# Kernel optimization log

Measured on AMD Instinct MI355X. Metric: run time of the kernel, lower is better.

## Reference

```python
import jax, jax.numpy as jnp
import numpy as np

N_HEADS = 3
DS_ITERS = 20
EPS = 1e-8
LN_EPS = 1e-5


def rmsnorm(x, w):
    rms = jnp.sqrt(jnp.mean(x * x, axis=-1, keepdims=True) + EPS)
    return x / rms * w


def layernorm(x, w, b):
    m = jnp.mean(x, axis=-1, keepdims=True)
    v = jnp.mean((x - m) ** 2, axis=-1, keepdims=True)
    return (x - m) / jnp.sqrt(v + LN_EPS) * w + b


def sinkhorn(m):
    # m: [b, t, n, n]; global max-shift then exp, 20 alternating row/col normalizations
    m = m - jnp.max(m, axis=(-2, -1), keepdims=True)
    m = jnp.exp(m)
    def body(_, m):
        m = m / (jnp.sum(m, axis=-1, keepdims=True) + EPS)
        m = m / (jnp.sum(m, axis=-2, keepdims=True) + EPS)
        return m
    return jax.lax.fori_loop(0, DS_ITERS, body, m)


def encoder_block(x, ln1_w, ln1_b, Wq, Wk, Wv, Wo, ln2_w, ln2_b, W1, W2):
    # Standard pre-norm ViT encoder block, bias=False, dropout inactive (eval)
    b, t, d = x.shape
    hd = d // N_HEADS
    h = layernorm(x, ln1_w, ln1_b)
    q = (h @ Wq).reshape(b, t, N_HEADS, hd)
    k = (h @ Wk).reshape(b, t, N_HEADS, hd)
    v = (h @ Wv).reshape(b, t, N_HEADS, hd)
    scores = jnp.einsum('bqhd,bkhd->bhqk', q, k) / jnp.sqrt(jnp.asarray(hd, x.dtype))
    attn = jax.nn.softmax(scores, axis=-1)
    o = jnp.einsum('bhqk,bkhd->bqhd', attn, v).reshape(b, t, d) @ Wo
    x = x + o
    h2 = layernorm(x, ln2_w, ln2_b)
    x = x + jax.nn.gelu(h2 @ W1) @ W2
    return x


def setup_inputs() -> dict:
    key = jax.random.key(0)
    ks = jax.random.split(key, 12)
    b, t, n, d = 32, 1024, 4, 192
    nd, mlp = n * d, 768
    std = 0.02
    x = jax.random.normal(ks[0], (b, t, n, d), dtype=jnp.float32)
    b_res = jnp.full((n, n), -10.0, dtype=jnp.float32)
    b_res = b_res.at[jnp.arange(n), jnp.arange(n)].set(0.0)
    return {
        'x': x,
        'norm_w': jnp.ones((nd,), jnp.float32),
        'phi_pre': std * jax.random.normal(ks[1], (nd, n), jnp.float32),
        'phi_post': std * jax.random.normal(ks[2], (nd, n), jnp.float32),
        'phi_res': std * jax.random.normal(ks[3], (nd, n * n), jnp.float32),
        'b_pre': jnp.full((n,), float(np.log(1.0 / (n - 1.0))), jnp.float32),
        'b_post': jnp.zeros((n,), jnp.float32),
        'b_res': b_res,
        'alpha_pre': jnp.asarray(0.001, jnp.float32),
        'alpha_post': jnp.asarray(0.001, jnp.float32),
        'alpha_res': jnp.asarray(0.001, jnp.float32),
        'ln1_w': jnp.ones((d,), jnp.float32),
        'ln1_b': jnp.zeros((d,), jnp.float32),
        'Wq': std * jax.random.normal(ks[4], (d, d), jnp.float32),
        'Wk': std * jax.random.normal(ks[5], (d, d), jnp.float32),
        'Wv': std * jax.random.normal(ks[6], (d, d), jnp.float32),
        'Wo': std * jax.random.normal(ks[7], (d, d), jnp.float32),
        'ln2_w': jnp.ones((d,), jnp.float32),
        'ln2_b': jnp.zeros((d,), jnp.float32),
        'W1': std * jax.random.normal(ks[8], (d, mlp), jnp.float32),
        'W2': std * jax.random.normal(ks[9], (mlp, d), jnp.float32),
    }


def reference(x, norm_w, phi_pre, phi_post, phi_res, b_pre, b_post, b_res,
              alpha_pre, alpha_post, alpha_res,
              ln1_w, ln1_b, Wq, Wk, Wv, Wo, ln2_w, ln2_b, W1, W2):
    b, t, n, d = x.shape
    streams = rmsnorm(x.reshape(b, t, n * d), norm_w)
    pre_tilde = alpha_pre * (streams @ phi_pre) + b_pre              # [b,t,n]
    post_tilde = alpha_post * (streams @ phi_post) + b_post         # [b,t,n]
    res_tilde = alpha_res * (streams @ phi_res) + b_res.reshape(1, 1, n * n)
    h_pre = jax.nn.sigmoid(pre_tilde)
    h_post = 2.0 * jax.nn.sigmoid(post_tilde)
    h_res = sinkhorn(res_tilde.reshape(b, t, n, n))                 # doubly stochastic
    x_res = jnp.einsum('btij,btjd->btid', h_res, x)
    x_in = jnp.einsum('btn,btnd->btd', h_pre, x)
    y = encoder_block(x_in, ln1_w, ln1_b, Wq, Wk, Wv, Wo, ln2_w, ln2_b, W1, W2)
    x_out = y[:, :, None, :] * h_post[..., None]
    return x_res + x_out
```

## Files before the change

### kernel.cpp

```cpp
#include <hip/hip_runtime.h>
#include <hip/hip_bf16.h>
#include <math.h>

#define BATCH 32
#define SEQ   1024
#define NS    4
#define DIM   192
#define ND    768
#define NH    3
#define HD    64
#define MLP   768
#define TOKENS (BATCH*SEQ)

typedef __bf16 bf16;
typedef bf16  bf16x8 __attribute__((ext_vector_type(8)));
typedef bf16  bf16x4 __attribute__((ext_vector_type(4)));
typedef float f32x4  __attribute__((ext_vector_type(4)));

#define MFMA16(a,b,c) __builtin_amdgcn_mfma_f32_16x16x32_bf16(a,b,c,0,0,0)
#define LOG2E 1.44269504088896f

__device__ inline float gelu_tanh(float x) {
    float x3 = x * x * x;
    return 0.5f * x * (1.0f + tanhf(0.7978845608028654f * (x + 0.044715f * x3)));
}

__global__ __launch_bounds__(256) void wprep_kernel(
    const float* __restrict__ Wq, const float* __restrict__ Wk,
    const float* __restrict__ Wv, const float* __restrict__ Wo,
    const float* __restrict__ W1, const float* __restrict__ W2,
    const float* __restrict__ nw, const float* __restrict__ ppre,
    const float* __restrict__ ppost, const float* __restrict__ pres,
    bf16* __restrict__ wqkv, bf16* __restrict__ wot,
    bf16* __restrict__ w1t, bf16* __restrict__ w2t, bf16* __restrict__ phiw)
{
    const int z = blockIdx.z;
    const int tid = blockIdx.x * 256 + threadIdx.x;
    if (z == 6) {
        if (tid >= 32 * 96) return;
        const int n = tid / 96, k8 = tid % 96;
        const int kch = k8 >> 2, quad = k8 & 3;
        const int ntile = n >> 4, nc = n & 15;
        bf16* d = phiw + ((size_t)(ntile * 24 + kch) * 64 + quad * 16 + nc) * 8;
#pragma unroll
        for (int e = 0; e < 8; e++) {
            const int k = k8 * 8 + e;
            float v;
            if      (n < 4)  v = ppre [k * 4  + n];
            else if (n < 8)  v = ppost[k * 4  + n - 4];
            else if (n < 24) v = pres [k * 16 + n - 8];
            else             v = 0.f;
            d[e] = (bf16)(nw[k] * v);
        }
        return;
    }
    const float* src; bf16* dst; int K, N; float scale = 1.f;
    switch (z) {
        case 0: src = Wq; dst = wqkv;            K = 192; N = 192;
                scale = 0.125f * LOG2E; break;
        case 1: src = Wk; dst = wqkv + 36864;    K = 192; N = 192; break;
        case 2: src = Wv; dst = wqkv + 73728;    K = 192; N = 192; break;
        case 3: src = Wo; dst = wot;             K = 192; N = 192; break;
        case 4: src = W1; dst = w1t;             K = 192; N = 768; break;
        default:src = W2; dst = w2t;             K = 768; N = 192; break;
    }
    const int K8 = K >> 3, KC = K >> 5;
    if (tid >= N * K8) return;
    const int n = tid / K8, k8 = tid % K8;
    const int kch = k8 >> 2, quad = k8 & 3;
    const int ntile = n >> 4, nc = n & 15;
    bf16* d = dst + ((size_t)(ntile * KC + kch) * 64 + quad * 16 + nc) * 8;
#pragma unroll
    for (int e = 0; e < 8; e++)
        d[e] = (bf16)(scale * src[(size_t)(k8 * 8 + e) * N + n]);
}

__global__ __launch_bounds__(64) void prep_kernel(
    const float* __restrict__ x, bf16* __restrict__ xb, float* __restrict__ rinv)
{
    const int tok = blockIdx.x, lane = threadIdx.x;
    const float* xt = x + (size_t)tok * ND;
    float4 xv[3];
    float ssq = 0.f;
#pragma unroll
    for (int r = 0; r < 3; r++) {
        xv[r] = ((const float4*)xt)[lane + 64 * r];
        ssq += xv[r].x*xv[r].x + xv[r].y*xv[r].y + xv[r].z*xv[r].z + xv[r].w*xv[r].w;
    }
#pragma unroll
    for (int off = 32; off; off >>= 1) ssq += __shfl_xor(ssq, off);
    if (lane == 0) rinv[tok] = rsqrtf(ssq / (float)ND + 1e-8f);
#pragma unroll
    for (int r = 0; r < 3; r++) {
        bf16x4 o = {(bf16)xv[r].x, (bf16)xv[r].y, (bf16)xv[r].z, (bf16)xv[r].w};
        *(bf16x4*)(xb + (size_t)tok * ND + 4 * (lane + 64 * r)) = o;
    }
}

__global__ __launch_bounds__(256) void dots_kernel(
    const bf16* __restrict__ xb, const bf16* __restrict__ phiw,
    const float* __restrict__ rinv, float* __restrict__ dots)
{
    const int tid = threadIdx.x, lane = tid & 63, w = tid >> 6;
    const int quad = lane >> 4, c = lane & 15;
    const int tok0 = blockIdx.x * 64 + w * 16;

    f32x4 acc0 = {0.f,0.f,0.f,0.f}, acc1 = {0.f,0.f,0.f,0.f};
    const bf16* arow = xb + (size_t)(tok0 + c) * ND + quad * 8;
    const bf16* bbase = phiw + lane * 8;
#pragma unroll 6
    for (int k0 = 0; k0 < ND; k0 += 32) {
        const int kch = k0 >> 5;
        bf16x8 af  = *(const bf16x8*)(arow + k0);
        bf16x8 bf0 = *(const bf16x8*)(bbase + (size_t)kch * 512);
        bf16x8 bf1 = *(const bf16x8*)(bbase + (size_t)(24 + kch) * 512);
        acc0 = MFMA16(af, bf0, acc0);
        acc1 = MFMA16(af, bf1, acc1);
    }
#pragma unroll
    for (int r = 0; r < 4; r++) {
        const int tok = tok0 + quad * 4 + r;
        const float s = rinv[tok];
        dots[(size_t)tok * 32 + c]      = acc0[r] * s;
        dots[(size_t)tok * 32 + 16 + c] = acc1[r] * s;
    }
}

__global__ __launch_bounds__(256) void sink_kernel(
    const float* __restrict__ dots, const float* __restrict__ b_pre,
    const float* __restrict__ b_post, const float* __restrict__ b_res,
    const float* __restrict__ a_pre, const float* __restrict__ a_post,
    const float* __restrict__ a_res,
    float* __restrict__ hgate, float* __restrict__ hpost)
{
    const int tok = blockIdx.x * 256 + threadIdx.x;
    const float* dt = dots + (size_t)tok * 32;
    float d[24];
#pragma unroll
    for (int i = 0; i < 6; i++) *(float4*)&d[i*4] = *(const float4*)(dt + i*4);

    const float apre = a_pre[0], apost = a_post[0], ares = a_res[0];
    float hpre[4], hpo[4], m[16];
#pragma unroll
    for (int i = 0; i < 4; i++) {
        hpre[i] = 1.f / (1.f + __expf(-(apre  * d[i]     + b_pre[i])));
        hpo[i]  = 2.f / (1.f + __expf(-(apost * d[4 + i] + b_post[i])));
    }
#pragma unroll
    for (int p = 0; p < 16; p++) m[p] = ares * d[8 + p] + b_res[p];

    float gm = m[0];
#pragma unroll
    for (int p = 1; p < 16; p++) gm = fmaxf(gm, m[p]);
#pragma unroll
    for (int p = 0; p < 16; p++) m[p] = __expf(m[p] - gm);

    for (int it = 0; it < 20; it++) {
#pragma unroll
        for (int i = 0; i < 4; i++) {
            const float inv = 1.f / (m[i*4+0] + m[i*4+1] + m[i*4+2] + m[i*4+3] + 1e-8f);
#pragma unroll
            for (int j = 0; j < 4; j++) m[i*4+j] *= inv;
        }
#pragma unroll
        for (int j = 0; j < 4; j++) {
            const float inv = 1.f / (m[0*4+j] + m[1*4+j] + m[2*4+j] + m[3*4+j] + 1e-8f);
#pragma unroll
            for (int i = 0; i < 4; i++) m[i*4+j] *= inv;
        }
    }

    float* hg = hgate + (size_t)tok * 20;
#pragma unroll
    for (int i = 0; i < 4; i++) *(float4*)(hg + i*4) = *(float4*)&m[i*4];
    *(float4*)(hg + 16) = *(float4*)hpre;
    *(float4*)(hpost + (size_t)tok * 4) = *(float4*)hpo;
}

__global__ __launch_bounds__(64) void mix_kernel(
    const bf16* __restrict__ xb, const float* __restrict__ hgate,
    const float* __restrict__ ln1_w, const float* __restrict__ ln1_b,
    float* __restrict__ xin, bf16* __restrict__ h1)
{
    const int tok = blockIdx.x, lane = threadIdx.x;
    __shared__ float ldsx[ND];

    const bf16* xt = xb + (size_t)tok * ND;
#pragma unroll
    for (int r = 0; r < 3; r++) {
        const bf16x4 v = *(const bf16x4*)(xt + 4 * (lane + 64 * r));
        float4 f = {(float)v[0], (float)v[1], (float)v[2], (float)v[3]};
        ((float4*)ldsx)[lane + 64 * r] = f;
    }

    const float* hg = hgate + (size_t)tok * 20 + 16;
    float hpre[4];
#pragma unroll
    for (int i = 0; i < 4; i++) hpre[i] = hg[i];

    __syncthreads();

    float xi[3];
#pragma unroll
    for (int r = 0; r < 3; r++) {
        const int d = lane + 64 * r;
        xi[r] = hpre[0]*ldsx[d] + hpre[1]*ldsx[DIM+d]
              + hpre[2]*ldsx[2*DIM+d] + hpre[3]*ldsx[3*DIM+d];
    }
    float sum = xi[0] + xi[1] + xi[2];
#pragma unroll
    for (int off = 32; off; off >>= 1) sum += __shfl_xor(sum, off);
    const float mean = sum / (float)DIM;
    float vs = (xi[0]-mean)*(xi[0]-mean) + (xi[1]-mean)*(xi[1]-mean) + (xi[2]-mean)*(xi[2]-mean);
#pragma unroll
    for (int off = 32; off; off >>= 1) vs += __shfl_xor(vs, off);
    const float inv = rsqrtf(vs / (float)DIM + 1e-5f);

    float* xint = xin + (size_t)tok * DIM;
    bf16*  ht   = h1  + (size_t)tok * DIM;
#pragma unroll
    for (int r = 0; r < 3; r++) {
        const int d = lane + 64 * r;
        xint[d] = xi[r];
        ht[d]   = (bf16)((xi[r] - mean) * inv * ln1_w[d] + ln1_b[d]);
    }
}

template<int EPI, int K>
__global__ __launch_bounds__(256) void gemm_bf(
    const bf16* __restrict__ A, const bf16* __restrict__ Bt,
    bf16* __restrict__ Cb, int N)
{
    const int tid = threadIdx.x, lane = tid & 63, w = tid >> 6;
    const int quad = lane >> 4, c = lane & 15;
    const int tok0 = blockIdx.y * 256 + w * 64;
    const int n0   = blockIdx.x * 64;
    const int KC   = K >> 5;

    f32x4 acc[4][4];
#pragma unroll
    for (int i = 0; i < 4; i++)
#pragma unroll
        for (int j = 0; j < 4; j++) acc[i][j] = (f32x4){0.f,0.f,0.f,0.f};

    const bf16* abase = A + (size_t)(tok0 + c) * K + quad * 8;
    const bf16* bbase = Bt + (size_t)(n0 >> 4) * KC * 512 + lane * 8;
#pragma unroll 2
    for (int k0 = 0; k0 < K; k0 += 32) {
        const int kch = k0 >> 5;
        bf16x8 af[4], bfr[4];
#pragma unroll
        for (int mt = 0; mt < 4; mt++)
            af[mt] = *(const bf16x8*)(abase + (size_t)mt * 16 * K + k0);
#pragma unroll
        for (int nt = 0; nt < 4; nt++)
            bfr[nt] = *(const bf16x8*)(bbase + (size_t)(nt * KC + kch) * 512);
#pragma unroll
        for (int mt = 0; mt < 4; mt++)
#pragma unroll
            for (int nt = 0; nt < 4; nt++)
                acc[mt][nt] = MFMA16(af[mt], bfr[nt], acc[mt][nt]);
    }

#pragma unroll
    for (int mt = 0; mt < 4; mt++)
#pragma unroll
        for (int r = 0; r < 4; r++) {
            const int row = tok0 + mt*16 + quad*4 + r;
#pragma unroll
            for (int nt = 0; nt < 4; nt++) {
                float v = acc[mt][nt][r];
                if (EPI == 2) v = gelu_tanh(v);
                Cb[(size_t)row * N + n0 + nt*16 + c] = (bf16)v;
            }
        }
}

__global__ __launch_bounds__(256) void gemm_wo_ln(
    const bf16* __restrict__ A, const bf16* __restrict__ Bt,
    const float* __restrict__ xin, const float* __restrict__ lw,
    const float* __restrict__ lb, float* __restrict__ x1, bf16* __restrict__ h2)
{
    const int tid = threadIdx.x, lane = tid & 63, w = tid >> 6;
    const int quad = lane >> 4, c = lane & 15;
    const int tok0 = blockIdx.x * 64 + w * 16;

    f32x4 acc[12];
#pragma unroll
    for (int j = 0; j < 12; j++) acc[j] = (f32x4){0.f,0.f,0.f,0.f};

    const bf16* abase = A + (size_t)(tok0 + c) * 192 + quad * 8;
    const bf16* bbase = Bt + lane * 8;
#pragma unroll 2
    for (int k0 = 0; k0 < 192; k0 += 32) {
        const int kch = k0 >> 5;
        bf16x8 af = *(const bf16x8*)(abase + k0);
#pragma unroll
        for (int nt = 0; nt < 12; nt++) {
            bf16x8 bfr = *(const bf16x8*)(bbase + (size_t)(nt * 6 + kch) * 512);
            acc[nt] = MFMA16(af, bfr, acc[nt]);
        }
    }

#pragma unroll
    for (int r = 0; r < 4; r++) {
        const int row = tok0 + quad*4 + r;
        float v[12], s = 0.f;
#pragma unroll
        for (int nt = 0; nt < 12; nt++) {
            v[nt] = acc[nt][r] + xin[(size_t)row * 192 + nt*16 + c];
            s += v[nt];
        }
#pragma unroll
        for (int off = 1; off < 16; off <<= 1) s += __shfl_xor(s, off);
        const float mean = s / 192.f;
        float vv = 0.f;
#pragma unroll
        for (int nt = 0; nt < 12; nt++) {
            const float d = v[nt] - mean;
            vv += d * d;
        }
#pragma unroll
        for (int off = 1; off < 16; off <<= 1) vv += __shfl_xor(vv, off);
        const float inv = rsqrtf(vv / 192.f + 1e-5f);
#pragma unroll
        for (int nt = 0; nt < 12; nt++) {
            const int col = nt*16 + c;
            x1[(size_t)row * 192 + col] = v[nt];
            h2[(size_t)row * 192 + col] = (bf16)((v[nt] - mean) * inv * lw[col] + lb[col]);
        }
    }
}

__global__ __launch_bounds__(256) void gemm_w2_final(
    const bf16* __restrict__ A, const bf16* __restrict__ Bt,
    const float* __restrict__ x1, const float* __restrict__ x,
    const float* __restrict__ hgate, const float* __restrict__ hpost,
    float* __restrict__ out)
{
    const int tid = threadIdx.x, lane = tid & 63, w = tid >> 6;
    const int quad = lane >> 4, c = lane & 15;
    const int tok0 = blockIdx.x * 64 + w * 16;
    const int s = blockIdx.y;

    f32x4 acc[4];
#pragma unroll
    for (int j = 0; j < 4; j++) acc[j] = (f32x4){0.f,0.f,0.f,0.f};

    const bf16* abase = A + (size_t)(tok0 + c) * 768 + quad * 8;
    const bf16* bbase = Bt + (size_t)(s * 4) * 24 * 512 + lane * 8;
#pragma unroll 4
    for (int k0 = 0; k0 < 768; k0 += 32) {
        const int kch = k0 >> 5;
        bf16x8 af = *(const bf16x8*)(abase + k0);
#pragma unroll
        for (int nt = 0; nt < 4; nt++) {
            bf16x8 bfr = *(const bf16x8*)(bbase + (size_t)(nt * 24 + kch) * 512);
            acc[nt] = MFMA16(af, bfr, acc[nt]);
        }
    }

#pragma unroll
    for (int r = 0; r < 4; r++) {
        const int row = tok0 + quad*4 + r;
        const float* hg = hgate + (size_t)row * 20;
        float hres[16];
#pragma unroll
        for (int p = 0; p < 16; p++) hres[p] = hg[p];
        const float4 hp = *(const float4*)(hpost + (size_t)row * 4);
        const float hpi[4] = {hp.x, hp.y, hp.z, hp.w};
        const float* xrow = x + (size_t)row * ND;
        float* orow = out + (size_t)row * ND;
#pragma unroll
        for (int nt = 0; nt < 4; nt++) {
            const int col = s*64 + nt*16 + c;
            const float y = acc[nt][r] + x1[(size_t)row * 192 + col];
            float xv[4];
#pragma unroll
            for (int j = 0; j < 4; j++) xv[j] = xrow[j * 192 + col];
#pragma unroll
            for (int i = 0; i < 4; i++) {
                const float xr = hres[i*4+0]*xv[0] + hres[i*4+1]*xv[1]
                               + hres[i*4+2]*xv[2] + hres[i*4+3]*xv[3];
                orow[i * 192 + col] = xr + y * hpi[i];
            }
        }
    }
}

__global__ __launch_bounds__(256) void vtrans_kernel(
    const bf16* __restrict__ qkv, bf16* __restrict__ vt)
{
    __shared__ bf16 t[64][72];
    const int tid = threadIdx.x;
    const int bh = blockIdx.y, b = bh / NH, h = bh % NH;
    const int s0 = blockIdx.x * 64;

#pragma unroll
    for (int i = 0; i < 2; i++) {
        const int chunk = tid + 256 * i;
        const int srow = chunk >> 3, g = chunk & 7;
        *(uint4*)&t[srow][g * 8] =
            *(const uint4*)(qkv + (size_t)(b * SEQ + s0 + srow) * 576 + 384 + h * 64 + g * 8);
    }
    __syncthreads();
#pragma unroll
    for (int i = 0; i < 2; i++) {
        const int chunk = tid + 256 * i;
        const int d = chunk >> 3, sg = chunk & 7;
        bf16x8 v;
#pragma unroll
        for (int j = 0; j < 8; j++) v[j] = t[sg * 8 + j][d];
        *(bf16x8*)(vt + ((size_t)bh * HD + d) * SEQ + s0 + sg * 8) = v;
    }
}

__global__ __launch_bounds__(64) void attn_mfma(
    const bf16* __restrict__ qkv, const bf16* __restrict__ vt,
    bf16* __restrict__ obuf)
{
    __shared__ bf16 Pw[32 * 64];
    const int lane = threadIdx.x;
    const int quad = lane >> 4, c = lane & 15;
    const int bh = blockIdx.y, b = bh / NH, h = bh % NH;
    const int q0 = blockIdx.x * 32;

    const bf16* kbase = qkv + (size_t)b * SEQ * 576 + 192 + h * 64;
    const bf16* vbase = vt + (size_t)bh * HD * SEQ;

    bf16x8 qf[2][2];
#pragma unroll
    for (int mt = 0; mt < 2; mt++)
#pragma unroll
        for (int ch = 0; ch < 2; ch++)
            qf[mt][ch] = *(const bf16x8*)(qkv + (size_t)(b * SEQ + q0 + mt*16 + c) * 576
                                              + h * 64 + ch * 32 + quad * 8);

    f32x4 of[2][4];
    float lst[2][4];
#pragma unroll
    for (int mt = 0; mt < 2; mt++)
#pragma unroll
        for (int r = 0; r < 4; r++) lst[mt][r] = 0.f;
#pragma unroll
    for (int mt = 0; mt < 2; mt++)
#pragma unroll
        for (int dt = 0; dt < 4; dt++) of[mt][dt] = (f32x4){0.f, 0.f, 0.f, 0.f};

#pragma unroll 1
    for (int kt = 0; kt < SEQ / 64; kt++) {
        f32x4 sf[2][4];
#pragma unroll
        for (int mt = 0; mt < 2; mt++)
#pragma unroll
            for (int nt = 0; nt < 4; nt++) sf[mt][nt] = (f32x4){0.f, 0.f, 0.f, 0.f};
#pragma unroll
        for (int ch = 0; ch < 2; ch++) {
            bf16x8 kf[4];
#pragma unroll
            for (int nt = 0; nt < 4; nt++)
                kf[nt] = *(const bf16x8*)(kbase + (size_t)(kt*64 + nt*16 + c) * 576
                                               + ch * 32 + quad * 8);
#pragma unroll
            for (int mt = 0; mt < 2; mt++)
#pragma unroll
                for (int nt = 0; nt < 4; nt++)
                    sf[mt][nt] = MFMA16(qf[mt][ch], kf[nt], sf[mt][nt]);
        }

#pragma unroll
        for (int mt = 0; mt < 2; mt++)
#pragma unroll
            for (int r = 0; r < 4; r++) {
                float rs = 0.f;
#pragma unroll
                for (int nt = 0; nt < 4; nt++) {
                    const float p = exp2f(sf[mt][nt][r]);
                    sf[mt][nt][r] = p;
                    rs += p;
                }
                lst[mt][r] += rs;
            }

#pragma unroll
        for (int mt = 0; mt < 2; mt++)
#pragma unroll
            for (int nt = 0; nt < 4; nt++)
#pragma unroll
                for (int r = 0; r < 4; r++) {
                    const int row = mt*16 + quad*4 + r;
                    const int col = nt*16 + c;
                    Pw[row*64 + (((col >> 3) ^ (row & 7)) * 8) + (col & 7)] =
                        (bf16)sf[mt][nt][r];
                }

#pragma unroll
        for (int ch = 0; ch < 2; ch++) {
            bf16x8 vf[4], pf[2];
#pragma unroll
            for (int dt = 0; dt < 4; dt++)
                vf[dt] = *(const bf16x8*)(vbase + (size_t)(dt*16 + c) * SEQ
                                               + kt*64 + ch*32 + quad*8);
#pragma unroll
            for (int mt = 0; mt < 2; mt++) {
                const int row = mt*16 + c;
                pf[mt] = *(const bf16x8*)(Pw + row*64 + (((ch*4 + quad) ^ (c & 7)) * 8));
            }
#pragma unroll
            for (int mt = 0; mt < 2; mt++)
#pragma unroll
                for (int dt = 0; dt < 4; dt++)
                    of[mt][dt] = MFMA16(pf[mt], vf[dt], of[mt][dt]);
        }
    }

#pragma unroll
    for (int mt = 0; mt < 2; mt++)
#pragma unroll
        for (int r = 0; r < 4; r++) {
            float s = lst[mt][r];
#pragma unroll
            for (int off = 1; off < 16; off <<= 1) s += __shfl_xor(s, off);
            const float inv = 1.0f / s;
            const size_t tok = (size_t)b * SEQ + q0 + mt*16 + quad*4 + r;
#pragma unroll
            for (int dt = 0; dt < 4; dt++)
                obuf[tok * DIM + h*64 + dt*16 + c] = (bf16)(of[mt][dt][r] * inv);
        }
}

extern "C" void kernel_launch(void* const* d_in, const int* in_sizes, int n_in,
                              void* d_out, int out_size, void* d_ws, size_t ws_size,
                              hipStream_t stream) {
    const float* x         = (const float*)d_in[0];
    const float* norm_w    = (const float*)d_in[1];
    const float* phi_pre   = (const float*)d_in[2];
    const float* phi_post  = (const float*)d_in[3];
    const float* phi_res   = (const float*)d_in[4];
    const float* b_pre     = (const float*)d_in[5];
    const float* b_post    = (const float*)d_in[6];
    const float* b_res     = (const float*)d_in[7];
    const float* alpha_pre = (const float*)d_in[8];
    const float* alpha_post= (const float*)d_in[9];
    const float* alpha_res = (const float*)d_in[10];
    const float* ln1_w     = (const float*)d_in[11];
    const float* ln1_b     = (const float*)d_in[12];
    const float* Wq        = (const float*)d_in[13];
    const float* Wk        = (const float*)d_in[14];
    const float* Wv        = (const float*)d_in[15];
    const float* Wo        = (const float*)d_in[16];
    const float* ln2_w     = (const float*)d_in[17];
    const float* ln2_b     = (const float*)d_in[18];
    const float* W1        = (const float*)d_in[19];
    const float* W2        = (const float*)d_in[20];

    float* out = (float*)d_out;
    float* ws  = (float*)d_ws;

    const size_t TBf = (size_t)TOKENS * DIM;
    float* xin   = ws;
    float* x1    = ws + TBf;
    float* hpost = ws + 2 * TBf;
    float* rinv  = hpost + 131072;
    float* hgate = rinv + 32768;
    bf16*  phiw  = (bf16*)(hgate + (size_t)TOKENS*20);
    bf16*  wqkv  = phiw + 24576;
    bf16*  wot   = wqkv + 110592;
    bf16*  w1t   = wot + 36864;
    bf16*  w2t   = w1t + 147456;
    float* regAC = (float*)(w2t + 147456);
    bf16*  xb    = (bf16*)regAC;
    bf16*  qkv   = (bf16*)regAC;
    bf16*  vt    = qkv + (size_t)TOKENS * 576;
    bf16*  gbuf  = (bf16*)regAC;
    float* regBD = regAC + 12582912;
    bf16*  h1    = (bf16*)regBD;
    bf16*  obuf  = h1;
    bf16*  h2    = h1 + TBf;
    float* dotsb = regBD + TBf / 2;

    wprep_kernel<<<dim3(72, 1, 7), 256, 0, stream>>>(
        Wq, Wk, Wv, Wo, W1, W2, norm_w, phi_pre, phi_post, phi_res,
        wqkv, wot, w1t, w2t, phiw);

    prep_kernel<<<TOKENS, 64, 0, stream>>>(x, xb, rinv);
    dots_kernel<<<TOKENS / 64, 256, 0, stream>>>(xb, phiw, rinv, dotsb);
    sink_kernel<<<TOKENS / 256, 256, 0, stream>>>(
        dotsb, b_pre, b_post, b_res, alpha_pre, alpha_post, alpha_res, hgate, hpost);
    mix_kernel<<<TOKENS, 64, 0, stream>>>(xb, hgate, ln1_w, ln1_b, xin, h1);

    gemm_bf<0, 192><<<dim3(576/64, TOKENS/256), 256, 0, stream>>>(h1, wqkv, qkv, 576);

    vtrans_kernel<<<dim3(SEQ/64, BATCH*NH), 256, 0, stream>>>(qkv, vt);

    attn_mfma<<<dim3(SEQ/32, BATCH*NH), 64, 0, stream>>>(qkv, vt, obuf);

    gemm_wo_ln<<<TOKENS/64, 256, 0, stream>>>(obuf, wot, xin, ln2_w, ln2_b, x1, h2);

    gemm_bf<2, 192><<<dim3(768/64, TOKENS/256), 256, 0, stream>>>(h2, w1t, gbuf, 768);

    gemm_w2_final<<<dim3(TOKENS/64, 3), 256, 0, stream>>>(
        gbuf, w2t, x1, x, hgate, hpost, out);
}
```

Before: 552.7 us.

## Split attention key loop across four waves and reduce partials in shared memory

After: 571.0 us. +3.3%, slower.

```diff
diff --git a/kernel.cpp b/kernel.cpp
--- a/kernel.cpp
+++ b/kernel.cpp
@@ -415,16 +415,20 @@
     }
 }
 
-__global__ __launch_bounds__(64) void attn_mfma(
+__global__ __launch_bounds__(256) void attn_mfma(
     const bf16* __restrict__ qkv, const bf16* __restrict__ vt,
     bf16* __restrict__ obuf)
 {
-    __shared__ bf16 Pw[32 * 64];
-    const int lane = threadIdx.x;
+    __shared__ float smem[8192];
+    __shared__ float lred[4][32];
+    const int tid  = threadIdx.x;
+    const int lane = tid & 63, w = tid >> 6;
     const int quad = lane >> 4, c = lane & 15;
     const int bh = blockIdx.y, b = bh / NH, h = bh % NH;
     const int q0 = blockIdx.x * 32;
 
+    bf16* Pw = (bf16*)smem + (size_t)w * 2048;
+
     const bf16* kbase = qkv + (size_t)b * SEQ * 576 + 192 + h * 64;
     const bf16* vbase = vt + (size_t)bh * HD * SEQ;
 
@@ -448,7 +452,7 @@
         for (int dt = 0; dt < 4; dt++) of[mt][dt] = (f32x4){0.f, 0.f, 0.f, 0.f};
 
 #pragma unroll 1
-    for (int kt = 0; kt < SEQ / 64; kt++) {
+    for (int kt = w * 4; kt < w * 4 + 4; kt++) {
         f32x4 sf[2][4];
 #pragma unroll
         for (int mt = 0; mt < 2; mt++)
@@ -521,12 +525,33 @@
             float s = lst[mt][r];
 #pragma unroll
             for (int off = 1; off < 16; off <<= 1) s += __shfl_xor(s, off);
-            const float inv = 1.0f / s;
-            const size_t tok = (size_t)b * SEQ + q0 + mt*16 + quad*4 + r;
-#pragma unroll
-            for (int dt = 0; dt < 4; dt++)
-                obuf[tok * DIM + h*64 + dt*16 + c] = (bf16)(of[mt][dt][r] * inv);
-        }
+            if (c == 0) lred[w][mt*16 + quad*4 + r] = s;
+        }
+
+    __syncthreads();
+
+#pragma unroll
+    for (int mt = 0; mt < 2; mt++)
+#pragma unroll
+        for (int dt = 0; dt < 4; dt++)
+#pragma unroll
+            for (int r = 0; r < 4; r++)
+                smem[w*2048 + (mt*16 + quad*4 + r)*64 + dt*16 + c] = of[mt][dt][r];
+
+    __syncthreads();
+
+    const int q  = tid >> 3;
+    const int d0 = (tid & 7) * 8;
+    const float linv = 1.f / (lred[0][q] + lred[1][q] + lred[2][q] + lred[3][q]);
+    const size_t tok = (size_t)b * SEQ + q0 + q;
+    bf16x8 o;
+#pragma unroll
+    for (int j = 0; j < 8; j++) {
+        const int idx = q*64 + d0 + j;
+        const float v = smem[idx] + smem[2048 + idx] + smem[4096 + idx] + smem[6144 + idx];
+        o[j] = (bf16)(v * linv);
+    }
+    *(bf16x8*)(obuf + tok * DIM + h * 64 + d0) = o;
 }
 
 extern "C" void kernel_launch(void* const* d_in, const int* in_sizes, int n_in,
@@ -593,7 +618,7 @@
 
     vtrans_kernel<<<dim3(SEQ/64, BATCH*NH), 256, 0, stream>>>(qkv, vt);
 
-    attn_mfma<<<dim3(SEQ/32, BATCH*NH), 64, 0, stream>>>(qkv, vt, obuf);
+    attn_mfma<<<dim3(SEQ/32, BATCH*NH), 256, 0, stream>>>(qkv, vt, obuf);
 
     gemm_wo_ln<<<TOKENS/64, 256, 0, stream>>>(obuf, wot, xin, ln2_w, ln2_b, x1, h2);
 
```
